# Kernel optimization log

Hardware: AMD Instinct MI355X
Metric: run time of the kernel (lower is better)

The kernel has to match this reference:

```python
import jax, jax.numpy as jnp
import numpy as np

V, D, CTX, NL = 32000, 1024, 2048, 2
B, T = 4, 2048
EPS = 1e-5


def _layer_norm(x, gamma, beta):
    mu = jnp.mean(x, axis=-1, keepdims=True)
    var = jnp.var(x, axis=-1, keepdims=True)  # biased, matches unbiased=False
    return gamma * (x - mu) / jnp.sqrt(var + EPS) + beta


def setup_inputs() -> dict:
    key = jax.random.key(0)
    ks = jax.random.split(key, 12)
    s = 0.02
    return {
        "x": jax.random.randint(ks[0], (B, T), 0, V),
        "emb": jax.random.normal(ks[1], (V, D), jnp.float32) * s,
        "pos": jax.random.normal(ks[2], (CTX, D), jnp.float32) * s,
        "wq": jax.random.normal(ks[3], (NL, D, D), jnp.float32) * s,
        "wk": jax.random.normal(ks[4], (NL, D, D), jnp.float32) * s,
        "wv": jax.random.normal(ks[5], (NL, D, D), jnp.float32) * s,
        "wo": jax.random.normal(ks[6], (NL, D, D), jnp.float32) * s,
        "wup": jax.random.normal(ks[7], (NL, D, 4 * D), jnp.float32) * s,
        "bup": jnp.zeros((NL, 4 * D), jnp.float32),
        "wdown": jax.random.normal(ks[8], (NL, 4 * D, D), jnp.float32) * s,
        "bdown": jnp.zeros((NL, D), jnp.float32),
        "ga": jnp.ones((NL, D), jnp.float32),
        "ba": jnp.zeros((NL, D), jnp.float32),
        "gm": jnp.ones((NL, D), jnp.float32),
        "bm": jnp.zeros((NL, D), jnp.float32),
    }


def reference(x, emb, pos, wq, wk, wv, wo, wup, bup, wdown, bdown, ga, ba, gm, bm):
    Bx, Tx = x.shape
    d_model = emb.shape[-1]
    inv_sqrt_d = 1.0 / jnp.sqrt(jnp.asarray(d_model, jnp.float32))
    h = emb[x] + pos[:Tx][None, :, :]           # [B,T,D]
    causal = jnp.tril(jnp.ones((Tx, Tx), bool))  # [T,T]
    neg_inf = jnp.asarray(-jnp.inf, h.dtype)
    n_layers = wq.shape[0]
    for l in range(n_layers):
        residual = h
        q = h @ wq[l]
        k = h @ wk[l]
        v = h @ wv[l]
        wei = jnp.einsum('btd,bsd->bts', q, k) * inv_sqrt_d  # [B,T,T]
        wei = jnp.where(causal[None], wei, neg_inf)
        attn = jax.nn.softmax(wei, axis=-1)
        out = jnp.einsum('bts,bsd->btd', attn, v)
        z = out @ wo[l]
        h = _layer_norm(residual + z, ga[l], ba[l])
        m = jax.nn.relu(h @ wup[l] + bup[l]) @ wdown[l] + bdown[l]
        h = _layer_norm(h + m, gm[l], bm[l])
    return h
```

## Files before the change

kernel.cpp:

```cpp
#include <hip/hip_runtime.h>
#include <stdint.h>

typedef unsigned short u16;
typedef short short8 __attribute__((ext_vector_type(8)));
typedef short short4v __attribute__((ext_vector_type(4)));
typedef float f32x4 __attribute__((ext_vector_type(4)));

#define DEV static __device__ __forceinline__

DEV u16 f2bf(float x) {
    union { float f; uint32_t u; } v; v.f = x;
    uint32_t r = v.u + 0x7FFFu + ((v.u >> 16) & 1u);
    return (u16)(r >> 16);
}
DEV float bf2f(u16 h) {
    union { uint32_t u; float f; } v; v.u = ((uint32_t)h) << 16;
    return v.f;
}

DEV void gload_lds16(const u16* g, u16* l) {
    __builtin_amdgcn_global_load_lds(
        (__attribute__((address_space(1))) void*)g,
        (__attribute__((address_space(3))) void*)l, 16, 0, 0);
}

enum { F_RELU = 1, F_ACCUM = 2, F_CSKIP = 4, F_CKLIM = 8 };

__global__ __launch_bounds__(256, 2)
void gemm_bt(const u16* __restrict__ A, const u16* __restrict__ B,
             float* __restrict__ Cf, u16* __restrict__ Cb,
             const float* __restrict__ bias,
             int M, int N, int K, int lda, int ldb, int ldc,
             long long sA, long long sB, long long sC,
             float scale, int flags)
{
    const int tm = blockIdx.x, tn = blockIdx.y, bz = blockIdx.z;
    if ((flags & F_CSKIP) && tn > tm) return;
    A += (long long)bz * sA;
    B += (long long)bz * sB;
    const long long coff = (long long)bz * sC;

    __shared__ u16 As[128 * 32];
    __shared__ u16 Bs[128 * 32];

    const int tid = threadIdx.x;
    const int lane = tid & 63, w = tid >> 6;
    const int wr = w >> 1, wc = w & 1;
    const int l15 = lane & 15, l4 = lane >> 4;

    f32x4 acc[4][4];
    const f32x4 z4 = {0.f, 0.f, 0.f, 0.f};
#pragma unroll
    for (int m = 0; m < 4; ++m)
#pragma unroll
        for (int n = 0; n < 4; ++n) acc[m][n] = z4;

    int kend = K;
    if (flags & F_CKLIM) { int ke = (tm + 1) * 128; if (ke < kend) kend = ke; }

    const u16* Abase = A + (long long)tm * 128 * lda;
    const u16* Bbase = B + (long long)tn * 128 * ldb;

    for (int k0 = 0; k0 < kend; k0 += 32) {
#pragma unroll
        for (int i = 0; i < 2; ++i) {
            const int e0 = (i * 4 + w) * 512;
            const int e  = e0 + lane * 8;
            const int row = e >> 5, col = e & 31;
            gload_lds16(Abase + (long long)row * lda + (k0 + col), (u16*)As + e0);
            gload_lds16(Bbase + (long long)row * ldb + (k0 + col), (u16*)Bs + e0);
        }
        __syncthreads();

        short8 af[4], bfr[4];
#pragma unroll
        for (int m = 0; m < 4; ++m)
            af[m] = *(const short8*)&As[(wr * 64 + m * 16 + l15) * 32 + l4 * 8];
#pragma unroll
        for (int n = 0; n < 4; ++n)
            bfr[n] = *(const short8*)&Bs[(wc * 64 + n * 16 + l15) * 32 + l4 * 8];
#pragma unroll
        for (int m = 0; m < 4; ++m)
#pragma unroll
            for (int n = 0; n < 4; ++n)
                acc[m][n] = __builtin_amdgcn_mfma_f32_16x16x32_bf16(af[m], bfr[n], acc[m][n], 0, 0, 0);
        __syncthreads();
    }

#pragma unroll
    for (int n = 0; n < 4; ++n) {
        const int c = tn * 128 + wc * 64 + n * 16 + l15;
        const float bv = bias ? bias[c] : 0.0f;
#pragma unroll
        for (int m = 0; m < 4; ++m) {
            const int r0 = tm * 128 + wr * 64 + m * 16 + l4 * 4;
#pragma unroll
            for (int j = 0; j < 4; ++j) {
                float v = acc[m][n][j] * scale + bv;
                if (flags & F_RELU) v = fmaxf(v, 0.0f);
                const long long off = coff + (long long)(r0 + j) * ldc + c;
                if (flags & F_ACCUM) v += Cf[off];
                if (Cf) Cf[off] = v;
                if (Cb) Cb[off] = f2bf(v);
            }
        }
    }
}

__global__ void transpose_f2b(const float* __restrict__ in, u16* __restrict__ out, int R, int C)
{
    __shared__ float tile[32][33];
    const int tx = threadIdx.x, ty = threadIdx.y;
    const int gx = blockIdx.x, gy = blockIdx.y;
#pragma unroll
    for (int i = 0; i < 4; ++i)
        tile[ty + i * 8][tx] = in[(long long)(gy * 32 + ty + i * 8) * C + gx * 32 + tx];
    __syncthreads();
#pragma unroll
    for (int i = 0; i < 4; ++i)
        out[(long long)(gx * 32 + ty + i * 8) * R + gy * 32 + tx] = f2bf(tile[tx][ty + i * 8]);
}

__global__ void transpose_b2b(const u16* __restrict__ in, u16* __restrict__ out,
                              int R, int C, long long sIn, long long sOut)
{
    __shared__ u16 tile[32][34];
    in  += (long long)blockIdx.z * sIn;
    out += (long long)blockIdx.z * sOut;
    const int tx = threadIdx.x, ty = threadIdx.y;
    const int gx = blockIdx.x, gy = blockIdx.y;
#pragma unroll
    for (int i = 0; i < 4; ++i)
        tile[ty + i * 8][tx] = in[(long long)(gy * 32 + ty + i * 8) * C + gx * 32 + tx];
    __syncthreads();
#pragma unroll
    for (int i = 0; i < 4; ++i)
        out[(long long)(gx * 32 + ty + i * 8) * R + gy * 32 + tx] = tile[tx][ty + i * 8];
}

__global__ __launch_bounds__(256)
void embed_kernel(const int* __restrict__ x, const float* __restrict__ emb,
                  const float* __restrict__ pos, float* __restrict__ h32, u16* __restrict__ hbf)
{
    const long long row = blockIdx.x;
    const int t = (int)(row & 2047);
    const int idx = x[row];
    const int tid = threadIdx.x;
    const float4 e = ((const float4*)(emb + (long long)idx * 1024))[tid];
    const float4 p = ((const float4*)(pos + (long long)t * 1024))[tid];
    float y0 = e.x + p.x, y1 = e.y + p.y, y2 = e.z + p.z, y3 = e.w + p.w;
    float4 o; o.x = y0; o.y = y1; o.z = y2; o.w = y3;
    ((float4*)(h32 + row * 1024))[tid] = o;
    short4v ob = { (short)f2bf(y0), (short)f2bf(y1), (short)f2bf(y2), (short)f2bf(y3) };
    *(short4v*)(hbf + row * 1024 + tid * 4) = ob;
}

__global__ __launch_bounds__(256)
void ln_kernel(const float* __restrict__ a, const float* __restrict__ b,
               const float* __restrict__ gamma, const float* __restrict__ beta,
               float* __restrict__ o32, u16* __restrict__ obf)
{
    const long long row = blockIdx.x;
    const int tid = threadIdx.x, lane = tid & 63, w = tid >> 6;
    const float4 xa = ((const float4*)(a + row * 1024))[tid];
    const float4 xb = ((const float4*)(b + row * 1024))[tid];
    float x0 = xa.x + xb.x, x1 = xa.y + xb.y, x2 = xa.z + xb.z, x3 = xa.w + xb.w;
    float s = x0 + x1 + x2 + x3;
    float q = x0 * x0 + x1 * x1 + x2 * x2 + x3 * x3;
#pragma unroll
    for (int o = 32; o; o >>= 1) { s += __shfl_xor(s, o, 64); q += __shfl_xor(q, o, 64); }
    __shared__ float red[8];
    if (lane == 0) { red[w] = s; red[4 + w] = q; }
    __syncthreads();
    s = red[0] + red[1] + red[2] + red[3];
    q = red[4] + red[5] + red[6] + red[7];
    const float mu = s * (1.0f / 1024.0f);
    const float var = q * (1.0f / 1024.0f) - mu * mu;
    const float rs = rsqrtf(var + 1e-5f);
    const float4 g  = ((const float4*)gamma)[tid];
    const float4 be = ((const float4*)beta)[tid];
    float y0 = (x0 - mu) * rs * g.x + be.x;
    float y1 = (x1 - mu) * rs * g.y + be.y;
    float y2 = (x2 - mu) * rs * g.z + be.z;
    float y3 = (x3 - mu) * rs * g.w + be.w;
    float4 o; o.x = y0; o.y = y1; o.z = y2; o.w = y3;
    ((float4*)(o32 + row * 1024))[tid] = o;
    short4v ob = { (short)f2bf(y0), (short)f2bf(y1), (short)f2bf(y2), (short)f2bf(y3) };
    *(short4v*)(obf + row * 1024 + tid * 4) = ob;
}

__global__ __launch_bounds__(256)
void softmax_causal(u16* __restrict__ SP)
{
    const long long row = blockIdx.x;
    const int t = (int)(row & 2047);
    u16* p = SP + row * 2048;
    const int tid = threadIdx.x, lane = tid & 63, w = tid >> 6;

    short8 v = *(const short8*)&p[tid * 8];
    float x[8];
#pragma unroll
    for (int j = 0; j < 8; ++j) {
        const int c = tid * 8 + j;
        x[j] = (c <= t) ? bf2f((u16)v[j]) : -1e30f;
    }
    float mx = x[0];
#pragma unroll
    for (int j = 1; j < 8; ++j) mx = fmaxf(mx, x[j]);
#pragma unroll
    for (int o = 32; o; o >>= 1) mx = fmaxf(mx, __shfl_xor(mx, o, 64));
    __shared__ float red[8];
    if (lane == 0) red[w] = mx;
    __syncthreads();
    mx = fmaxf(fmaxf(red[0], red[1]), fmaxf(red[2], red[3]));

    float s = 0.f;
#pragma unroll
    for (int j = 0; j < 8; ++j) {
        const float e = (tid * 8 + j <= t) ? exp2f((x[j] - mx) * 1.44269504f) : 0.f;
        x[j] = e; s += e;
    }
#pragma unroll
    for (int o = 32; o; o >>= 1) s += __shfl_xor(s, o, 64);
    if (lane == 0) red[4 + w] = s;
    __syncthreads();
    s = red[4] + red[5] + red[6] + red[7];
    const float inv = 1.0f / s;

    short8 ov;
#pragma unroll
    for (int j = 0; j < 8; ++j) ov[j] = (short)f2bf(x[j] * inv);
    *(short8*)&p[tid * 8] = ov;
}

extern "C" void kernel_launch(void* const* d_in, const int* in_sizes, int n_in,
                              void* d_out, int out_size, void* d_ws, size_t ws_size,
                              hipStream_t stream)
{
    (void)in_sizes; (void)n_in; (void)out_size; (void)ws_size;
    const int Dd = 1024, T_ = 2048, B_ = 4, NLl = 2, M = B_ * T_;
    const float inv_sqrt_d = 0.03125f;

    const int*   x     = (const int*)  d_in[0];
    const float* emb   = (const float*)d_in[1];
    const float* pos   = (const float*)d_in[2];
    const float* wq    = (const float*)d_in[3];
    const float* wk    = (const float*)d_in[4];
    const float* wv    = (const float*)d_in[5];
    const float* wo    = (const float*)d_in[6];
    const float* wup   = (const float*)d_in[7];
    const float* bup   = (const float*)d_in[8];
    const float* wdown = (const float*)d_in[9];
    const float* bdown = (const float*)d_in[10];
    const float* ga    = (const float*)d_in[11];
    const float* ba    = (const float*)d_in[12];
    const float* gm    = (const float*)d_in[13];
    const float* bm    = (const float*)d_in[14];

    char* ws = (char*)d_ws;
    size_t off = 0;
    auto alloc = [&](size_t bytes) -> void* {
        void* p = ws + off; off += (bytes + 255) & ~(size_t)255; return p;
    };
    float* h32  = (float*)alloc((size_t)M * Dd * 4);
    u16*   hbf  = (u16*)  alloc((size_t)M * Dd * 2);
    float* z32  = (float*)alloc((size_t)M * Dd * 4);
    u16*   qbf  = (u16*)  alloc((size_t)M * Dd * 2);
    u16*   kbf  = (u16*)  alloc((size_t)M * Dd * 2);
    u16*   vbf  = (u16*)  alloc((size_t)M * Dd * 2);
    u16*   vtbf = (u16*)  alloc((size_t)M * Dd * 2);
    u16*   SP   = (u16*)  alloc((size_t)B_ * T_ * T_ * 2);
    u16*   ubf  = (u16*)  alloc((size_t)M * 2048 * 2);
    u16*   wtb  = (u16*)  alloc((size_t)12 * 1024 * 1024 * 2);

    u16* wq_t    = wtb;
    u16* wk_t    = wtb + 1 * 1048576;
    u16* wv_t    = wtb + 2 * 1048576;
    u16* wo_t    = wtb + 3 * 1048576;
    u16* wup_t   = wtb + 4 * 1048576;
    u16* wdown_t = wtb + 8 * 1048576;

    dim3 blk(256);
    dim3 tblk(32, 8);

    embed_kernel<<<M, blk, 0, stream>>>(x, emb, pos, h32, hbf);

    for (int l = 0; l < NLl; ++l) {
        const float* wq_l    = wq    + (size_t)l * Dd * Dd;
        const float* wk_l    = wk    + (size_t)l * Dd * Dd;
        const float* wv_l    = wv    + (size_t)l * Dd * Dd;
        const float* wo_l    = wo    + (size_t)l * Dd * Dd;
        const float* wup_l   = wup   + (size_t)l * Dd * 4096;
        const float* wdown_l = wdown + (size_t)l * 4096 * Dd;

        transpose_f2b<<<dim3(32, 32),  tblk, 0, stream>>>(wq_l, wq_t, 1024, 1024);
        transpose_f2b<<<dim3(32, 32),  tblk, 0, stream>>>(wk_l, wk_t, 1024, 1024);
        transpose_f2b<<<dim3(32, 32),  tblk, 0, stream>>>(wv_l, wv_t, 1024, 1024);
        transpose_f2b<<<dim3(32, 32),  tblk, 0, stream>>>(wo_l, wo_t, 1024, 1024);
        transpose_f2b<<<dim3(128, 32), tblk, 0, stream>>>(wup_l, wup_t, 1024, 4096);
        transpose_f2b<<<dim3(32, 128), tblk, 0, stream>>>(wdown_l, wdown_t, 4096, 1024);

        gemm_bt<<<dim3(64, 8, 1), blk, 0, stream>>>(hbf, wq_t, nullptr, qbf, nullptr,
            M, 1024, 1024, 1024, 1024, 1024, 0, 0, 0, inv_sqrt_d, 0);
        gemm_bt<<<dim3(64, 8, 1), blk, 0, stream>>>(hbf, wk_t, nullptr, kbf, nullptr,
            M, 1024, 1024, 1024, 1024, 1024, 0, 0, 0, 1.0f, 0);
        gemm_bt<<<dim3(64, 8, 1), blk, 0, stream>>>(hbf, wv_t, nullptr, vbf, nullptr,
            M, 1024, 1024, 1024, 1024, 1024, 0, 0, 0, 1.0f, 0);

        transpose_b2b<<<dim3(32, 64, 4), tblk, 0, stream>>>(vbf, vtbf, 2048, 1024,
            (long long)T_ * Dd, (long long)T_ * Dd);

        gemm_bt<<<dim3(16, 16, 4), blk, 0, stream>>>(qbf, kbf, nullptr, SP, nullptr,
            2048, 2048, 1024, 1024, 1024, 2048,
            (long long)T_ * Dd, (long long)T_ * Dd, (long long)T_ * T_, 1.0f, F_CSKIP);

        softmax_causal<<<B_ * T_, blk, 0, stream>>>(SP);

        gemm_bt<<<dim3(16, 8, 4), blk, 0, stream>>>(SP, vtbf, nullptr, qbf, nullptr,
            2048, 1024, 2048, 2048, 2048, 1024,
            (long long)T_ * T_, (long long)Dd * T_, (long long)T_ * Dd, 1.0f, F_CKLIM);

        gemm_bt<<<dim3(64, 8, 1), blk, 0, stream>>>(qbf, wo_t, z32, nullptr, nullptr,
            M, 1024, 1024, 1024, 1024, 1024, 0, 0, 0, 1.0f, 0);

        ln_kernel<<<M, blk, 0, stream>>>(h32, z32, ga + (size_t)l * Dd, ba + (size_t)l * Dd, h32, hbf);

        for (int c = 0; c < 2; ++c) {
            gemm_bt<<<dim3(64, 16, 1), blk, 0, stream>>>(hbf, wup_t + (size_t)c * 2048 * 1024,
                nullptr, ubf, bup + (size_t)l * 4096 + c * 2048,
                M, 2048, 1024, 1024, 1024, 2048, 0, 0, 0, 1.0f, F_RELU);
            gemm_bt<<<dim3(64, 8, 1), blk, 0, stream>>>(ubf, wdown_t + (size_t)c * 2048,
                z32, nullptr, (c == 0) ? (bdown + (size_t)l * Dd) : nullptr,
                M, 1024, 2048, 2048, 4096, 1024, 0, 0, 0, 1.0f, (c == 0) ? 0 : F_ACCUM);
        }

        float* lnout = (l == NLl - 1) ? (float*)d_out : h32;
        ln_kernel<<<M, blk, 0, stream>>>(h32, z32, gm + (size_t)l * Dd, bm + (size_t)l * Dd, lnout, hbf);
    }
}
```

Measured before the change: 1.259 ms.

## Add 256x256 8-wave GEMM kernel, fuse QKV projection, unsplit MLP up-projection

Adds a new 512-thread GEMM kernel with 256x256 output tiles, double-buffered swizzled LDS staging via direct global-to-LDS loads, and interleaved MFMA quadrants. Q, K and V weights are concatenated so one GEMM produces a strided QKV buffer, with the softmax scale folded into the Wq transpose. The MLP up-projection now runs as a single N=4096 GEMM instead of two chunks with accumulation. The goal is more data reuse per tile and fewer launches, at the cost of a larger intermediate buffer and strided attention inputs.

After: 1.202 ms. 4.5% less time.

```diff
diff --git a/kernel.cpp b/kernel.cpp
--- a/kernel.cpp
+++ b/kernel.cpp
@@ -107,7 +107,142 @@
     }
 }
 
-__global__ void transpose_f2b(const float* __restrict__ in, u16* __restrict__ out, int R, int C)
+
+DEV void stage_half(const u16* __restrict__ g, int ld, u16* l, int tid) {
+#pragma unroll
+    for (int i = 0; i < 2; ++i) {
+        const int oe = (i * 512 + tid) * 8;
+        const int row = oe >> 6;
+        const int c = (oe & 63) ^ ((row & 7) << 3);
+        gload_lds16(g + (long long)row * ld + c, l + (i * 512 + (tid & ~63)) * 8);
+    }
+}
+
+#define BAR() do { __builtin_amdgcn_s_barrier(); __builtin_amdgcn_sched_barrier(0); } while (0)
+#define WAIT_LGKM0() do { asm volatile("s_waitcnt lgkmcnt(0)" ::: "memory"); __builtin_amdgcn_sched_barrier(0); } while (0)
+
+#define READ_A(H) do {                                                        \
+    const u16* _b = As_ + ((t & 1) * 2 + (H)) * 8192;                         \
+    _Pragma("unroll") for (int rb = 0; rb < 4; ++rb)                          \
+    _Pragma("unroll") for (int ks = 0; ks < 2; ++ks) {                        \
+        const int _row = wm * 64 + rb * 16 + l15;                             \
+        const int _k = ks * 32 + l4 * 8;                                      \
+        af[rb * 2 + ks] = *(const short8*)(_b + _row * 64 + (_k ^ ((_row & 7) << 3))); \
+    } } while (0)
+
+#define READ_B(H) do {                                                        \
+    const u16* _b = Bs_ + ((t & 1) * 2 + (H)) * 8192;                         \
+    _Pragma("unroll") for (int cb2 = 0; cb2 < 2; ++cb2)                       \
+    _Pragma("unroll") for (int ks = 0; ks < 2; ++ks) {                        \
+        const int _col = wn * 32 + cb2 * 16 + l15;                            \
+        const int _k = ks * 32 + l4 * 8;                                      \
+        bf[cb2 * 2 + ks] = *(const short8*)(_b + _col * 64 + (_k ^ ((_col & 7) << 3))); \
+    } } while (0)
+
+#define MFMA_Q(QM, QN) do {                                                   \
+    __builtin_amdgcn_s_setprio(1);                                            \
+    _Pragma("unroll") for (int rb = 0; rb < 4; ++rb)                          \
+    _Pragma("unroll") for (int cb2 = 0; cb2 < 2; ++cb2)                       \
+    _Pragma("unroll") for (int ks = 0; ks < 2; ++ks)                          \
+        acc[QM][rb][QN][cb2] = __builtin_amdgcn_mfma_f32_16x16x32_bf16(       \
+            af[rb * 2 + ks], bf[cb2 * 2 + ks], acc[QM][rb][QN][cb2], 0, 0, 0);\
+    __builtin_amdgcn_s_setprio(0);                                            \
+    } while (0)
+
+#define STAGE_A(T, H) stage_half(Abase + (long long)((H) * 128) * lda + (T) * 64, lda, \
+                                 As_ + (((T) & 1) * 2 + (H)) * 8192, tid)
+#define STAGE_B(T, H) stage_half(Bbase + (long long)((H) * 128) * ldb + (T) * 64, ldb, \
+                                 Bs_ + (((T) & 1) * 2 + (H)) * 8192, tid)
+
+__global__ __launch_bounds__(512, 2)
+void gemm_bt8(const u16* __restrict__ A, const u16* __restrict__ B,
+              u16* __restrict__ Cb, const float* __restrict__ bias,
+              int M, int N, int K, int lda, int ldb, int ldc, int flags)
+{
+    __shared__ u16 lds[65536];
+    u16* As_ = lds;
+    u16* Bs_ = lds + 32768;
+
+    const int tid = threadIdx.x;
+    const int lane = tid & 63, w = tid >> 6;
+    const int wm = w >> 2, wn = w & 3;
+    const int tm = blockIdx.x, tn = blockIdx.y;
+    const int l15 = lane & 15, l4 = lane >> 4;
+
+    const u16* Abase = A + (long long)tm * 256 * lda;
+    const u16* Bbase = B + (long long)tn * 256 * ldb;
+    const int nt = K >> 6;
+
+    f32x4 acc[2][4][2][2];
+    const f32x4 z4 = {0.f, 0.f, 0.f, 0.f};
+#pragma unroll
+    for (int a = 0; a < 2; ++a)
+#pragma unroll
+        for (int b = 0; b < 4; ++b)
+#pragma unroll
+            for (int c = 0; c < 2; ++c)
+#pragma unroll
+                for (int d = 0; d < 2; ++d) acc[a][b][c][d] = z4;
+
+    STAGE_A(0, 0); STAGE_B(0, 0); STAGE_A(0, 1); STAGE_B(0, 1);
+    if (nt > 1) {
+        STAGE_A(1, 0); STAGE_B(1, 0);
+        asm volatile("s_waitcnt vmcnt(4)" ::: "memory");
+    } else {
+        asm volatile("s_waitcnt vmcnt(0)" ::: "memory");
+    }
+    BAR();
+
+    short8 af[8], bf[4];
+    for (int t = 0; t < nt; ++t) {
+        READ_A(0); READ_B(0);
+        if (t + 1 < nt) STAGE_A(t + 1, 1);
+        BAR(); WAIT_LGKM0();
+        MFMA_Q(0, 0);
+        BAR();
+        READ_B(1);
+        if (t + 1 < nt) STAGE_B(t + 1, 1);
+        BAR(); WAIT_LGKM0();
+        MFMA_Q(0, 1);
+        BAR();
+        READ_A(1); READ_B(0);
+        if (t + 2 < nt) STAGE_A(t + 2, 0);
+        BAR(); WAIT_LGKM0();
+        MFMA_Q(1, 0);
+        BAR();
+        READ_B(1);
+        if (t + 2 < nt) STAGE_B(t + 2, 0);
+        BAR(); WAIT_LGKM0();
+        MFMA_Q(1, 1);
+        if (t + 2 < nt) { asm volatile("s_waitcnt vmcnt(4)" ::: "memory"); }
+        else            { asm volatile("s_waitcnt vmcnt(0)" ::: "memory"); }
+        BAR();
+    }
+
+#pragma unroll
+    for (int qn2 = 0; qn2 < 2; ++qn2)
+#pragma unroll
+    for (int cb2 = 0; cb2 < 2; ++cb2) {
+        const int c = tn * 256 + qn2 * 128 + wn * 32 + cb2 * 16 + l15;
+        const float bv = bias ? bias[c] : 0.0f;
+#pragma unroll
+        for (int qm2 = 0; qm2 < 2; ++qm2)
+#pragma unroll
+        for (int rb = 0; rb < 4; ++rb) {
+            const int r0 = tm * 256 + qm2 * 128 + wm * 64 + rb * 16 + l4 * 4;
+#pragma unroll
+            for (int j = 0; j < 4; ++j) {
+                float v = acc[qm2][rb][qn2][cb2][j] + bv;
+                if (flags & F_RELU) v = fmaxf(v, 0.0f);
+                Cb[(long long)(r0 + j) * ldc + c] = f2bf(v);
+            }
+        }
+    }
+}
+
+
+__global__ void transpose_f2b(const float* __restrict__ in, u16* __restrict__ out,
+                              int R, int C, float scale)
 {
     __shared__ float tile[32][33];
     const int tx = threadIdx.x, ty = threadIdx.y;
@@ -118,11 +253,11 @@
     __syncthreads();
 #pragma unroll
     for (int i = 0; i < 4; ++i)
-        out[(long long)(gx * 32 + ty + i * 8) * R + gy * 32 + tx] = f2bf(tile[tx][ty + i * 8]);
+        out[(long long)(gx * 32 + ty + i * 8) * R + gy * 32 + tx] = f2bf(tile[tx][ty + i * 8] * scale);
 }
 
 __global__ void transpose_b2b(const u16* __restrict__ in, u16* __restrict__ out,
-                              int R, int C, long long sIn, long long sOut)
+                              int R, int C, int ldin, long long sIn, long long sOut)
 {
     __shared__ u16 tile[32][34];
     in  += (long long)blockIdx.z * sIn;
@@ -131,7 +266,7 @@
     const int gx = blockIdx.x, gy = blockIdx.y;
 #pragma unroll
     for (int i = 0; i < 4; ++i)
-        tile[ty + i * 8][tx] = in[(long long)(gy * 32 + ty + i * 8) * C + gx * 32 + tx];
+        tile[ty + i * 8][tx] = in[(long long)(gy * 32 + ty + i * 8) * ldin + gx * 32 + tx];
     __syncthreads();
 #pragma unroll
     for (int i = 0; i < 4; ++i)
@@ -262,25 +397,21 @@
     auto alloc = [&](size_t bytes) -> void* {
         void* p = ws + off; off += (bytes + 255) & ~(size_t)255; return p;
     };
-    float* h32  = (float*)alloc((size_t)M * Dd * 4);
-    u16*   hbf  = (u16*)  alloc((size_t)M * Dd * 2);
-    float* z32  = (float*)alloc((size_t)M * Dd * 4);
-    u16*   qbf  = (u16*)  alloc((size_t)M * Dd * 2);
-    u16*   kbf  = (u16*)  alloc((size_t)M * Dd * 2);
-    u16*   vbf  = (u16*)  alloc((size_t)M * Dd * 2);
-    u16*   vtbf = (u16*)  alloc((size_t)M * Dd * 2);
-    u16*   SP   = (u16*)  alloc((size_t)B_ * T_ * T_ * 2);
-    u16*   ubf  = (u16*)  alloc((size_t)M * 2048 * 2);
-    u16*   wtb  = (u16*)  alloc((size_t)12 * 1024 * 1024 * 2);
-
-    u16* wq_t    = wtb;
-    u16* wk_t    = wtb + 1 * 1048576;
-    u16* wv_t    = wtb + 2 * 1048576;
-    u16* wo_t    = wtb + 3 * 1048576;
-    u16* wup_t   = wtb + 4 * 1048576;
-    u16* wdown_t = wtb + 8 * 1048576;
+    float* h32   = (float*)alloc((size_t)M * Dd * 4);
+    u16*   hbf   = (u16*)  alloc((size_t)M * Dd * 2);
+    float* z32   = (float*)alloc((size_t)M * Dd * 4);
+    u16*   qkv   = (u16*)  alloc((size_t)M * 3072 * 2);
+    u16*   abf   = (u16*)  alloc((size_t)M * Dd * 2);
+    u16*   vtbf  = (u16*)  alloc((size_t)M * Dd * 2);
+    u16*   SP    = (u16*)  alloc((size_t)B_ * T_ * T_ * 2);
+    u16*   ubf   = (u16*)  alloc((size_t)M * 4096 * 2);
+    u16*   wqkv_t  = (u16*)alloc((size_t)3072 * 1024 * 2);
+    u16*   wo_t    = (u16*)alloc((size_t)1024 * 1024 * 2);
+    u16*   wup_t   = (u16*)alloc((size_t)4096 * 1024 * 2);
+    u16*   wdown_t = (u16*)alloc((size_t)1024 * 4096 * 2);
 
     dim3 blk(256);
+    dim3 blk8(512);
     dim3 tblk(32, 8);
 
     embed_kernel<<<M, blk, 0, stream>>>(x, emb, pos, h32, hbf);
@@ -293,46 +424,40 @@
         const float* wup_l   = wup   + (size_t)l * Dd * 4096;
         const float* wdown_l = wdown + (size_t)l * 4096 * Dd;
 
-        transpose_f2b<<<dim3(32, 32),  tblk, 0, stream>>>(wq_l, wq_t, 1024, 1024);
-        transpose_f2b<<<dim3(32, 32),  tblk, 0, stream>>>(wk_l, wk_t, 1024, 1024);
-        transpose_f2b<<<dim3(32, 32),  tblk, 0, stream>>>(wv_l, wv_t, 1024, 1024);
-        transpose_f2b<<<dim3(32, 32),  tblk, 0, stream>>>(wo_l, wo_t, 1024, 1024);
-        transpose_f2b<<<dim3(128, 32), tblk, 0, stream>>>(wup_l, wup_t, 1024, 4096);
-        transpose_f2b<<<dim3(32, 128), tblk, 0, stream>>>(wdown_l, wdown_t, 4096, 1024);
-
-        gemm_bt<<<dim3(64, 8, 1), blk, 0, stream>>>(hbf, wq_t, nullptr, qbf, nullptr,
-            M, 1024, 1024, 1024, 1024, 1024, 0, 0, 0, inv_sqrt_d, 0);
-        gemm_bt<<<dim3(64, 8, 1), blk, 0, stream>>>(hbf, wk_t, nullptr, kbf, nullptr,
-            M, 1024, 1024, 1024, 1024, 1024, 0, 0, 0, 1.0f, 0);
-        gemm_bt<<<dim3(64, 8, 1), blk, 0, stream>>>(hbf, wv_t, nullptr, vbf, nullptr,
-            M, 1024, 1024, 1024, 1024, 1024, 0, 0, 0, 1.0f, 0);
-
-        transpose_b2b<<<dim3(32, 64, 4), tblk, 0, stream>>>(vbf, vtbf, 2048, 1024,
-            (long long)T_ * Dd, (long long)T_ * Dd);
-
-        gemm_bt<<<dim3(16, 16, 4), blk, 0, stream>>>(qbf, kbf, nullptr, SP, nullptr,
-            2048, 2048, 1024, 1024, 1024, 2048,
-            (long long)T_ * Dd, (long long)T_ * Dd, (long long)T_ * T_, 1.0f, F_CSKIP);
+        transpose_f2b<<<dim3(32, 32),  tblk, 0, stream>>>(wq_l, wqkv_t,               1024, 1024, inv_sqrt_d);
+        transpose_f2b<<<dim3(32, 32),  tblk, 0, stream>>>(wk_l, wqkv_t + 1024 * 1024, 1024, 1024, 1.0f);
+        transpose_f2b<<<dim3(32, 32),  tblk, 0, stream>>>(wv_l, wqkv_t + 2048 * 1024, 1024, 1024, 1.0f);
+        transpose_f2b<<<dim3(32, 32),  tblk, 0, stream>>>(wo_l, wo_t, 1024, 1024, 1.0f);
+        transpose_f2b<<<dim3(128, 32), tblk, 0, stream>>>(wup_l, wup_t, 1024, 4096, 1.0f);
+        transpose_f2b<<<dim3(32, 128), tblk, 0, stream>>>(wdown_l, wdown_t, 4096, 1024, 1.0f);
+
+        gemm_bt8<<<dim3(32, 12), blk8, 0, stream>>>(hbf, wqkv_t, qkv, nullptr,
+            M, 3072, 1024, 1024, 1024, 3072, 0);
+
+        transpose_b2b<<<dim3(32, 64, 4), tblk, 0, stream>>>(qkv + 2048, vtbf, 2048, 1024,
+            3072, (long long)T_ * 3072, (long long)Dd * T_);
+
+        gemm_bt<<<dim3(16, 16, 4), blk, 0, stream>>>(qkv, qkv + 1024, nullptr, SP, nullptr,
+            2048, 2048, 1024, 3072, 3072, 2048,
+            (long long)T_ * 3072, (long long)T_ * 3072, (long long)T_ * T_, 1.0f, F_CSKIP);
 
         softmax_causal<<<B_ * T_, blk, 0, stream>>>(SP);
 
-        gemm_bt<<<dim3(16, 8, 4), blk, 0, stream>>>(SP, vtbf, nullptr, qbf, nullptr,
+        gemm_bt<<<dim3(16, 8, 4), blk, 0, stream>>>(SP, vtbf, nullptr, abf, nullptr,
             2048, 1024, 2048, 2048, 2048, 1024,
             (long long)T_ * T_, (long long)Dd * T_, (long long)T_ * Dd, 1.0f, F_CKLIM);
 
-        gemm_bt<<<dim3(64, 8, 1), blk, 0, stream>>>(qbf, wo_t, z32, nullptr, nullptr,
+        gemm_bt<<<dim3(64, 8, 1), blk, 0, stream>>>(abf, wo_t, z32, nullptr, nullptr,
             M, 1024, 1024, 1024, 1024, 1024, 0, 0, 0, 1.0f, 0);
 
         ln_kernel<<<M, blk, 0, stream>>>(h32, z32, ga + (size_t)l * Dd, ba + (size_t)l * Dd, h32, hbf);
 
-        for (int c = 0; c < 2; ++c) {
-            gemm_bt<<<dim3(64, 16, 1), blk, 0, stream>>>(hbf, wup_t + (size_t)c * 2048 * 1024,
-                nullptr, ubf, bup + (size_t)l * 4096 + c * 2048,
-                M, 2048, 1024, 1024, 1024, 2048, 0, 0, 0, 1.0f, F_RELU);
-            gemm_bt<<<dim3(64, 8, 1), blk, 0, stream>>>(ubf, wdown_t + (size_t)c * 2048,
-                z32, nullptr, (c == 0) ? (bdown + (size_t)l * Dd) : nullptr,
-                M, 1024, 2048, 2048, 4096, 1024, 0, 0, 0, 1.0f, (c == 0) ? 0 : F_ACCUM);
-        }
+        gemm_bt8<<<dim3(32, 16), blk8, 0, stream>>>(hbf, wup_t, ubf, bup + (size_t)l * 4096,
+            M, 4096, 1024, 1024, 1024, 4096, F_RELU);
+
+        gemm_bt<<<dim3(64, 8, 1), blk, 0, stream>>>(ubf, wdown_t, z32, nullptr,
+            bdown + (size_t)l * Dd,
+            M, 1024, 4096, 4096, 4096, 1024, 0, 0, 0, 1.0f, 0);
 
         float* lnout = (l == NLl - 1) ? (float*)d_out : h32;
         ln_kernel<<<M, blk, 0, stream>>>(h32, z32, gm + (size_t)l * Dd, bm + (size_t)l * Dd, lnout, hbf);
```
